# Kernel tuning notes

Hardware: AMD Instinct MI355X
Metric: run time of the kernel (lower is better)

## Reference

```python
import jax, jax.numpy as jnp
import numpy as np

B, T, D, H = 8192, 128, 16, 32
EPS = 1e-5  # BatchNorm1d default eps (eval mode, running stats)


def setup_inputs() -> dict:
    key = jax.random.key(0)
    ks = iter(jax.random.split(key, 64))

    def nrm(shape, s=0.1):
        return jax.random.normal(next(ks), shape, jnp.float32) * s

    inp = {}
    inp["S"] = nrm((B, T, D), 1.0)
    inp["g_S"] = nrm((B, T), 1.0)
    inp["times"] = jnp.linspace(0.0, 1.0, T, dtype=jnp.float32)
    inp["payoff_T"] = nrm((B,), 1.0)
    inp["delta_T"] = nrm((B, D), 1.0)
    # init_hidden: uniform(-0.1, 0.1), shape [num_layers=2, B, H]
    inp["h_price0"] = jax.random.uniform(next(ks), (2, B, H), jnp.float32, -0.1, 0.1)
    inp["h_delta0"] = jax.random.uniform(next(ks), (2, B, H), jnp.float32, -0.1, 0.1)
    # params for price net (prefix p_, out_dim=1) and delta net (prefix d_, out_dim=D)
    for pfx, out_dim in (("p", 1), ("d", D)):
        inp[pfx + "_Wih0"] = nrm((3 * H, 2 * D))
        inp[pfx + "_Whh0"] = nrm((3 * H, H))
        inp[pfx + "_bih0"] = nrm((3 * H,))
        inp[pfx + "_bhh0"] = nrm((3 * H,))
        inp[pfx + "_Wih1"] = nrm((3 * H, H))
        inp[pfx + "_Whh1"] = nrm((3 * H, H))
        inp[pfx + "_bih1"] = nrm((3 * H,))
        inp[pfx + "_bhh1"] = nrm((3 * H,))
        inp[pfx + "_embW"] = nrm((H, H))
        inp[pfx + "_embB"] = nrm((H,))
        inp[pfx + "_bng"] = jnp.ones((H,), jnp.float32)
        inp[pfx + "_bnb"] = jnp.zeros((H,), jnp.float32)
        inp[pfx + "_bnm"] = nrm((H,))
        inp[pfx + "_bnv"] = jax.random.uniform(next(ks), (H,), jnp.float32, 0.5, 1.5)
        inp[pfx + "_outW"] = nrm((out_dim, H))
        inp[pfx + "_outB"] = nrm((out_dim,))
    return inp


def _gru_cell(x, h, Wih, Whh, bih, bhh):
    # PyTorch GRU cell, gate order (r, z, n)
    gi = x @ Wih.T + bih
    gh = h @ Whh.T + bhh
    ir, iz, inn = jnp.split(gi, 3, axis=-1)
    hr, hz, hn = jnp.split(gh, 3, axis=-1)
    r = jax.nn.sigmoid(ir + hr)
    z = jax.nn.sigmoid(iz + hz)
    n = jnp.tanh(inn + r * hn)
    return (1.0 - z) * n + z * h


def _head(y, Wemb, bemb, g, b, m, v, Wout, bout, sig):
    # Linear -> BatchNorm1d (eval, running stats) -> SiLU -> Linear [-> Sigmoid]
    e = y @ Wemb.T + bemb
    e = (e - m) * jax.lax.rsqrt(v + EPS) * g + b
    e = e * jax.nn.sigmoid(e)  # SiLU
    o = e @ Wout.T + bout
    return jax.nn.sigmoid(o) if sig else o


def reference(S, g_S, times, payoff_T, delta_T, h_price0, h_delta0,
              p_Wih0, p_Whh0, p_bih0, p_bhh0, p_Wih1, p_Whh1, p_bih1, p_bhh1,
              p_embW, p_embB, p_bng, p_bnb, p_bnm, p_bnv, p_outW, p_outB,
              d_Wih0, d_Whh0, d_bih0, d_bhh0, d_Wih1, d_Whh1, d_bih1, d_bhh1,
              d_embW, d_embB, d_bng, d_bnb, d_bnm, d_bnv, d_outW, d_outB):
    # X = cat([S, g_S expanded to d]) -> [B, T, 2D]
    gS = jnp.broadcast_to(g_S[..., None], S.shape)
    X = jnp.concatenate([S, gS], axis=-1)
    Xr = jnp.swapaxes(X, 0, 1)[::-1]  # [T, B, 2D], time reversed (loop goes t=T-1..0)

    def step(carry, xt):
        hp0, hp1, hd0, hd1 = carry
        hp0 = _gru_cell(xt, hp0, p_Wih0, p_Whh0, p_bih0, p_bhh0)
        hp1 = _gru_cell(hp0, hp1, p_Wih1, p_Whh1, p_bih1, p_bhh1)
        hd0 = _gru_cell(xt, hd0, d_Wih0, d_Whh0, d_bih0, d_bhh0)
        hd1 = _gru_cell(hd0, hd1, d_Wih1, d_Whh1, d_bih1, d_bhh1)
        return (hp0, hp1, hd0, hd1), (hp1, hd1)

    carry0 = (h_price0[0], h_price0[1], h_delta0[0], h_delta0[1])
    _, (Yp, Yd) = jax.lax.scan(step, carry0, Xr)
    # flip time back to forward order: outputs were collected for t=T-1..0
    Yp = jnp.swapaxes(Yp[::-1], 0, 1)  # [B, T, H]
    Yd = jnp.swapaxes(Yd[::-1], 0, 1)  # [B, T, H]
    prices = _head(Yp, p_embW, p_embB, p_bng, p_bnb, p_bnm, p_bnv, p_outW, p_outB, False)  # [B,T,1]
    deltas = _head(Yd, d_embW, d_embB, d_bng, d_bnb, d_bnm, d_bnv, d_outW, d_outB, True)   # [B,T,D]
    return (prices, deltas)
```

## Files before the change

### kernel.cpp

```cpp
#include <hip/hip_runtime.h>
#include <hip/hip_bf16.h>
#include <stdint.h>

#define DI __device__ __forceinline__

typedef float f32x4 __attribute__((ext_vector_type(4)));
typedef short bf16x8 __attribute__((ext_vector_type(8)));

constexpr int BB = 8192, TT = 128, DD = 16, HH = 32;
constexpr float kEPS = 1e-5f;
constexpr float kLOG2E = 1.44269504088896340736f;

DI float rcpf_(float x) { return __builtin_amdgcn_rcpf(x); }
DI float exp2f_(float x) { return __builtin_amdgcn_exp2f(x); }
DI float sig_pre(float acc) { return rcpf_(1.0f + exp2f_(acc)); }
DI float sigm(float x) { return rcpf_(1.0f + exp2f_(-kLOG2E * x)); }

DI uint32_t cvtpk(float lo, float hi) {
  uint32_t r;
  asm("v_cvt_pk_bf16_f32 %0, %1, %2" : "=v"(r) : "v"(lo), "v"(hi));
  return r;
}

DI f32x4 mfma_(bf16x8 a, bf16x8 b, f32x4 c) {
  return __builtin_amdgcn_mfma_f32_16x16x32_bf16(a, b, c, 0, 0, 0);
}

DI void barrier_lds() {
  asm volatile("s_waitcnt lgkmcnt(0)" ::: "memory");
  __builtin_amdgcn_s_barrier();
  asm volatile("" ::: "memory");
}

union U4 { uint4 q; bf16x8 v; };

__global__ void prep_net(const float* Wih0, const float* Whh0,
                         const float* bih0, const float* bhh0,
                         const float* Wih1, const float* Whh1,
                         const float* bih1, const float* bhh1,
                         const float* embW, const float* embB,
                         const float* bng, const float* bnb,
                         const float* bnm, const float* bnv,
                         const float* outW, const float* outB,
                         int outDim, uint8_t* wsbase) {
  int tid = threadIdx.x;
  uint16_t* W = (uint16_t*)wsbase;
  float* bias = (float*)(wsbase + 27648);
  auto cvt = [](float f) -> uint16_t {
    union { float f; uint32_t u; } v; v.f = f;
    uint32_t u = v.u;
    return (uint16_t)((u + 0x7FFF + ((u >> 16) & 1)) >> 16);
  };
  for (int idx = tid; idx < 27 * 64; idx += 256) {
    int tile = idx >> 6, l = idx & 63, cc = l & 15, gg = l >> 4;
    uint16_t* dst = W + (size_t)idx * 8;
    if (tile < 24) {
      const float* mats[4] = {Wih0, Whh0, Wih1, Whh1};
      const float* src = mats[tile / 6];
      int sub = tile % 6;
      int row = sub * 16 + cc;
      float sc = (sub < 4) ? -kLOG2E : 2.0f * kLOG2E;
#pragma unroll
      for (int j = 0; j < 8; ++j) dst[j] = cvt(src[row * 32 + 8 * gg + j] * sc);
    } else if (tile < 26) {
      int row = (tile - 24) * 16 + cc;
      float a = bng[row] * rsqrtf(bnv[row] + kEPS);
#pragma unroll
      for (int j = 0; j < 8; ++j) dst[j] = cvt(embW[row * 32 + 8 * gg + j] * a);
    } else {
      int rrow = (cc < outDim) ? cc : 0;
      float sc = (cc < outDim) ? 1.0f : 0.0f;
#pragma unroll
      for (int j = 0; j < 8; ++j) dst[j] = cvt(outW[rrow * 32 + 8 * gg + j] * sc);
    }
  }
  for (int idx = tid; idx < 304; idx += 256) {
    int tile = idx >> 4, n = idx & 15;
    float v;
    if (tile < 8) {
      if (tile < 4)      v = (bih0[tile * 16 + n] + bhh0[tile * 16 + n]) * (-kLOG2E);
      else if (tile < 6) v = bih0[64 + (tile - 4) * 16 + n] * (2.0f * kLOG2E);
      else               v = bhh0[64 + (tile - 6) * 16 + n] * (2.0f * kLOG2E);
    } else if (tile < 16) {
      int tt = tile - 8;
      if (tt < 4)        v = (bih1[tt * 16 + n] + bhh1[tt * 16 + n]) * (-kLOG2E);
      else if (tt < 6)   v = bih1[64 + (tt - 4) * 16 + n] * (2.0f * kLOG2E);
      else               v = bhh1[64 + (tt - 6) * 16 + n] * (2.0f * kLOG2E);
    } else if (tile < 18) {
      int nn = (tile - 16) * 16 + n;
      float a = bng[nn] * rsqrtf(bnv[nn] + kEPS);
      v = a * (embB[nn] - bnm[nn]) + bnb[nn];
    } else {
      v = (n < outDim) ? outB[n] : 0.0f;
    }
    bias[idx] = v;
  }
}

__global__ __launch_bounds__(128, 2) void rnn_fused(
    const float* __restrict__ S, const float* __restrict__ gS,
    const float* __restrict__ hp0, const float* __restrict__ hd0,
    const uint8_t* __restrict__ ws, float* __restrict__ out) {
  const int tid = threadIdx.x, lane = tid & 63, wid = tid >> 6;
  const int net = blockIdx.x & 1;
  const int b0 = (blockIdx.x >> 1) * 16;
  const int c = lane & 15, g = lane >> 4;

  const uint16_t* W = (const uint16_t*)(ws + net * 32768);
  const float* bias = (const float*)(ws + net * 32768 + 27648);
  const float* hsrc = net ? hd0 : hp0;

  __shared__ uint4 sl[2][64];

  const int addr0 = ((lane & 15) | ((lane & 16) << 1)) << 2;
  const int addr1 = addr0 + 64;
  const bool lo32 = lane < 32;
  auto regroup = [&](const float (&v)[8]) -> bf16x8 {
    int P0 = (int)cvtpk(v[0], v[1]), P1 = (int)cvtpk(v[2], v[3]);
    int Q0 = (int)cvtpk(v[4], v[5]), Q1 = (int)cvtpk(v[6], v[7]);
    union { uint32_t u[4]; bf16x8 r; } t;
    int a, b;
    a = __builtin_amdgcn_ds_bpermute(addr0, P0);
    b = __builtin_amdgcn_ds_bpermute(addr0, Q0);
    t.u[0] = lo32 ? a : b;
    a = __builtin_amdgcn_ds_bpermute(addr0, P1);
    b = __builtin_amdgcn_ds_bpermute(addr0, Q1);
    t.u[1] = lo32 ? a : b;
    a = __builtin_amdgcn_ds_bpermute(addr1, P0);
    b = __builtin_amdgcn_ds_bpermute(addr1, Q0);
    t.u[2] = lo32 ? a : b;
    a = __builtin_amdgcn_ds_bpermute(addr1, P1);
    b = __builtin_amdgcn_ds_bpermute(addr1, Q1);
    t.u[3] = lo32 ? a : b;
    return t.r;
  };

  auto gruStep = [&](const bf16x8 (&Wi)[6], const bf16x8 (&Wh)[6],
                     const f32x4 (&Bb)[8], bf16x8 xf, bf16x8 hf,
                     float (&hC)[8]) {
    f32x4 r0 = mfma_(Wi[0], xf, Bb[0]); r0 = mfma_(Wh[0], hf, r0);
    f32x4 r1 = mfma_(Wi[1], xf, Bb[1]); r1 = mfma_(Wh[1], hf, r1);
    f32x4 z0 = mfma_(Wi[2], xf, Bb[2]); z0 = mfma_(Wh[2], hf, z0);
    f32x4 z1 = mfma_(Wi[3], xf, Bb[3]); z1 = mfma_(Wh[3], hf, z1);
    f32x4 ni0 = mfma_(Wi[4], xf, Bb[4]);
    f32x4 ni1 = mfma_(Wi[5], xf, Bb[5]);
    f32x4 nh0 = mfma_(Wh[4], hf, Bb[6]);
    f32x4 nh1 = mfma_(Wh[5], hf, Bb[7]);
#pragma unroll
    for (int r = 0; r < 4; ++r) {
      float rg0 = sig_pre(r0[r]), rg1 = sig_pre(r1[r]);
      float zg0 = sig_pre(z0[r]), zg1 = sig_pre(z1[r]);
      float w0 = ni0[r] + rg0 * nh0[r];
      float w1 = ni1[r] + rg1 * nh1[r];
      float n0 = 1.0f - 2.0f * rcpf_(1.0f + exp2f_(w0));
      float n1 = 1.0f - 2.0f * rcpf_(1.0f + exp2f_(w1));
      hC[r]     = n0 + zg0 * (hC[r]     - n0);
      hC[4 + r] = n1 + zg1 * (hC[4 + r] - n1);
    }
  };

  auto mkB = [&](const float* row) -> bf16x8 {
    f32x4 a = *(const f32x4*)(row);
    f32x4 b = *(const f32x4*)(row + 4);
    union { uint32_t u[4]; bf16x8 v; } t;
    t.u[0] = cvtpk(a[0], a[1]); t.u[1] = cvtpk(a[2], a[3]);
    t.u[2] = cvtpk(b[0], b[1]); t.u[3] = cvtpk(b[2], b[3]);
    return t.v;
  };

  if (wid == 0) {
    bf16x8 Wi[6], Wh[6];
#pragma unroll
    for (int t = 0; t < 6; ++t) {
      Wi[t] = *(const bf16x8*)(W + ((0 + t) * 64 + lane) * 8);
      Wh[t] = *(const bf16x8*)(W + ((6 + t) * 64 + lane) * 8);
    }
    f32x4 Bb[8];
#pragma unroll
    for (int t = 0; t < 8; ++t)
      Bb[t] = *(const f32x4*)(bias + t * 16 + 4 * g);

    float h0C[8];
#pragma unroll
    for (int r = 0; r < 4; ++r) {
      h0C[r]     = hsrc[(size_t)(b0 + c) * HH + 4 * g + r];
      h0C[4 + r] = hsrc[(size_t)(b0 + c) * HH + 16 + 4 * g + r];
    }
    bf16x8 h0B = mkB(hsrc + (size_t)(b0 + c) * HH + 8 * g);

    auto mkX = [&](f32x4 sa, f32x4 sb, float gs) -> bf16x8 {
      uint32_t pkg = cvtpk(gs, gs);
      union { uint32_t u[4]; bf16x8 v; } t;
      uint32_t p0 = cvtpk(sa[0], sa[1]), p1 = cvtpk(sa[2], sa[3]);
      uint32_t p2 = cvtpk(sb[0], sb[1]), p3 = cvtpk(sb[2], sb[3]);
      t.u[0] = lo32 ? p0 : pkg;
      t.u[1] = lo32 ? p1 : pkg;
      t.u[2] = lo32 ? p2 : pkg;
      t.u[3] = lo32 ? p3 : pkg;
      return t.v;
    };

    const float* Sp  = S  + ((size_t)(b0 + c) * TT + (TT - 1)) * DD + 8 * (g & 1);
    const float* gSp = gS + (size_t)(b0 + c) * TT + (TT - 1);
    f32x4 sa = *(const f32x4*)Sp, sb = *(const f32x4*)(Sp + 4);
    float gs = *gSp;

    bf16x8 xB = mkX(sa, sb, gs);
    gruStep(Wi, Wh, Bb, xB, h0B, h0C);
    h0B = regroup(h0C);
    { U4 u; u.v = h0B; sl[0][lane] = u.q; }
    Sp -= DD; gSp -= 1;
    sa = *(const f32x4*)Sp; sb = *(const f32x4*)(Sp + 4); gs = *gSp;
    barrier_lds();

#pragma unroll 1
    for (int i = 1; i < TT; ++i) {
      xB = mkX(sa, sb, gs);
      const float* Spn  = (i < TT - 1) ? Sp - DD : Sp;
      const float* gSpn = (i < TT - 1) ? gSp - 1 : gSp;
      sa = *(const f32x4*)Spn; sb = *(const f32x4*)(Spn + 4); gs = *gSpn;
      Sp = Spn; gSp = gSpn;

      gruStep(Wi, Wh, Bb, xB, h0B, h0C);
      h0B = regroup(h0C);
      { U4 u; u.v = h0B; sl[i & 1][lane] = u.q; }
      barrier_lds();
    }
  } else {
    bf16x8 Wi[6], Wh[6], We0, We1, Wo;
#pragma unroll
    for (int t = 0; t < 6; ++t) {
      Wi[t] = *(const bf16x8*)(W + ((12 + t) * 64 + lane) * 8);
      Wh[t] = *(const bf16x8*)(W + ((18 + t) * 64 + lane) * 8);
    }
    We0 = *(const bf16x8*)(W + (24 * 64 + lane) * 8);
    We1 = *(const bf16x8*)(W + (25 * 64 + lane) * 8);
    Wo  = *(const bf16x8*)(W + (26 * 64 + lane) * 8);
    f32x4 Bb[8];
#pragma unroll
    for (int t = 0; t < 8; ++t)
      Bb[t] = *(const f32x4*)(bias + (8 + t) * 16 + 4 * g);
    const f32x4 Be0 = *(const f32x4*)(bias + 16 * 16 + 4 * g);
    const f32x4 Be1 = *(const f32x4*)(bias + 17 * 16 + 4 * g);
    const f32x4 Bo  = *(const f32x4*)(bias + 18 * 16 + 4 * g);

    float h1C[8];
#pragma unroll
    for (int r = 0; r < 4; ++r) {
      h1C[r]     = hsrc[((size_t)BB + b0 + c) * HH + 4 * g + r];
      h1C[4 + r] = hsrc[((size_t)BB + b0 + c) * HH + 16 + 4 * g + r];
    }
    bf16x8 h1B = mkB(hsrc + ((size_t)BB + b0 + c) * HH + 8 * g);

    auto head = [&](bf16x8 h1f, int th) {
      f32x4 e0 = mfma_(We0, h1f, Be0);
      f32x4 e1 = mfma_(We1, h1f, Be1);
      float es[8];
#pragma unroll
      for (int r = 0; r < 4; ++r) {
        float a = e0[r], b = e1[r];
        es[r]     = a * sigm(a);
        es[4 + r] = b * sigm(b);
      }
      bf16x8 ef = regroup(es);
      f32x4 o = mfma_(Wo, ef, Bo);
      if (net == 0) {
        if (lane < 16) out[(size_t)(b0 + c) * TT + th] = o[0];
      } else {
        f32x4 so;
#pragma unroll
        for (int r = 0; r < 4; ++r) so[r] = sigm(o[r]);
        *(f32x4*)(out + (size_t)BB * TT +
                  ((size_t)(b0 + c) * TT + th) * DD + 4 * g) = so;
      }
    };

    barrier_lds();
#pragma unroll 1
    for (int i = 1; i < TT; ++i) {
      U4 u; u.q = sl[(i - 1) & 1][lane];
      bf16x8 h0t = u.v;
      gruStep(Wi, Wh, Bb, h0t, h1B, h1C);
      h1B = regroup(h1C);
      head(h1B, TT - i);
      barrier_lds();
    }
    U4 u; u.q = sl[1][lane];
    gruStep(Wi, Wh, Bb, u.v, h1B, h1C);
    h1B = regroup(h1C);
    head(h1B, 0);
  }
}

extern "C" void kernel_launch(void* const* d_in, const int* in_sizes, int n_in,
                              void* d_out, int out_size, void* d_ws,
                              size_t ws_size, hipStream_t stream) {
  const float* S   = (const float*)d_in[0];
  const float* gS  = (const float*)d_in[1];
  const float* hp0 = (const float*)d_in[5];
  const float* hd0 = (const float*)d_in[6];
  uint8_t* ws = (uint8_t*)d_ws;

  prep_net<<<1, 256, 0, stream>>>(
      (const float*)d_in[7],  (const float*)d_in[8],  (const float*)d_in[9],
      (const float*)d_in[10], (const float*)d_in[11], (const float*)d_in[12],
      (const float*)d_in[13], (const float*)d_in[14], (const float*)d_in[15],
      (const float*)d_in[16], (const float*)d_in[17], (const float*)d_in[18],
      (const float*)d_in[19], (const float*)d_in[20], (const float*)d_in[21],
      (const float*)d_in[22], 1, ws);
  prep_net<<<1, 256, 0, stream>>>(
      (const float*)d_in[23], (const float*)d_in[24], (const float*)d_in[25],
      (const float*)d_in[26], (const float*)d_in[27], (const float*)d_in[28],
      (const float*)d_in[29], (const float*)d_in[30], (const float*)d_in[31],
      (const float*)d_in[32], (const float*)d_in[33], (const float*)d_in[34],
      (const float*)d_in[35], (const float*)d_in[36], (const float*)d_in[37],
      (const float*)d_in[38], 16, ws + 32768);

  rnn_fused<<<dim3((BB / 16) * 2), dim3(128), 0, stream>>>(S, gS, hp0, hd0,
                                                           ws, (float*)d_out);
}
```

Baseline: 157.3 us.

## Split GRU layers and head into three warp-specialized pipeline stages with LDS rings

The block grows from two to three wavefronts. Wave 0 runs layer 0, wave 1 runs layer 1, and a new wave 2 runs the embedding/BN/SiLU/output head. They hand data through 8-deep LDS ring buffers. Each stage processes four timesteps between barriers, so there are fewer barriers and the head's matmuls and stores come off the layer-1 critical path. Wave 0 also batches its S and gS loads for four steps at once. The cost is more threads per block and more LDS, which changes occupancy, plus a two-epoch pipeline fill and drain.

```diff
diff --git a/kernel.cpp b/kernel.cpp
--- a/kernel.cpp
+++ b/kernel.cpp
@@ -97,7 +97,9 @@
   }
 }
 
-__global__ __launch_bounds__(128, 2) void rnn_fused(
+constexpr int KE = 4;
+constexpr int NE = TT / KE;
+__global__ __launch_bounds__(192, 3) void rnn_fused(
     const float* __restrict__ S, const float* __restrict__ gS,
     const float* __restrict__ hp0, const float* __restrict__ hd0,
     const uint8_t* __restrict__ ws, float* __restrict__ out) {
@@ -110,7 +112,8 @@
   const float* bias = (const float*)(ws + net * 32768 + 27648);
   const float* hsrc = net ? hd0 : hp0;
 
-  __shared__ uint4 sl[2][64];
+  __shared__ uint4 ring0[8][64];
+  __shared__ uint4 ring1[8][64];
 
   const int addr0 = ((lane & 15) | ((lane & 16) << 1)) << 2;
   const int addr1 = addr0 + 64;
@@ -200,57 +203,76 @@
       return t.v;
     };
 
-    const float* Sp  = S  + ((size_t)(b0 + c) * TT + (TT - 1)) * DD + 8 * (g & 1);
-    const float* gSp = gS + (size_t)(b0 + c) * TT + (TT - 1);
-    f32x4 sa = *(const f32x4*)Sp, sb = *(const f32x4*)(Sp + 4);
-    float gs = *gSp;
-
-    bf16x8 xB = mkX(sa, sb, gs);
-    gruStep(Wi, Wh, Bb, xB, h0B, h0C);
-    h0B = regroup(h0C);
-    { U4 u; u.v = h0B; sl[0][lane] = u.q; }
-    Sp -= DD; gSp -= 1;
-    sa = *(const f32x4*)Sp; sb = *(const f32x4*)(Sp + 4); gs = *gSp;
-    barrier_lds();
+    const float* Sbase  = S  + (size_t)(b0 + c) * TT * DD + 8 * (g & 1);
+    const float* gSbase = gS + (size_t)(b0 + c) * TT;
 
 #pragma unroll 1
-    for (int i = 1; i < TT; ++i) {
-      xB = mkX(sa, sb, gs);
-      const float* Spn  = (i < TT - 1) ? Sp - DD : Sp;
-      const float* gSpn = (i < TT - 1) ? gSp - 1 : gSp;
-      sa = *(const f32x4*)Spn; sb = *(const f32x4*)(Spn + 4); gs = *gSpn;
-      Sp = Spn; gSp = gSpn;
-
-      gruStep(Wi, Wh, Bb, xB, h0B, h0C);
-      h0B = regroup(h0C);
-      { U4 u; u.v = h0B; sl[i & 1][lane] = u.q; }
+    for (int e = 0; e < NE + 2; ++e) {
+      if (e < NE) {
+        const int sg0 = KE * e;
+        f32x4 sa[KE], sb[KE];
+        float gv[KE];
+#pragma unroll
+        for (int s = 0; s < KE; ++s) {
+          int t = TT - 1 - (sg0 + s);
+          const float* p = Sbase + (size_t)t * DD;
+          sa[s] = *(const f32x4*)p;
+          sb[s] = *(const f32x4*)(p + 4);
+          gv[s] = gSbase[t];
+        }
+#pragma unroll
+        for (int s = 0; s < KE; ++s) {
+          bf16x8 xB = mkX(sa[s], sb[s], gv[s]);
+          gruStep(Wi, Wh, Bb, xB, h0B, h0C);
+          h0B = regroup(h0C);
+          U4 u; u.v = h0B;
+          ring0[(sg0 + s) & 7][lane] = u.q;
+        }
+      }
       barrier_lds();
     }
-  } else {
-    bf16x8 Wi[6], Wh[6], We0, We1, Wo;
+  } else if (wid == 1) {
+    bf16x8 Wi[6], Wh[6];
 #pragma unroll
     for (int t = 0; t < 6; ++t) {
       Wi[t] = *(const bf16x8*)(W + ((12 + t) * 64 + lane) * 8);
       Wh[t] = *(const bf16x8*)(W + ((18 + t) * 64 + lane) * 8);
     }
-    We0 = *(const bf16x8*)(W + (24 * 64 + lane) * 8);
-    We1 = *(const bf16x8*)(W + (25 * 64 + lane) * 8);
-    Wo  = *(const bf16x8*)(W + (26 * 64 + lane) * 8);
     f32x4 Bb[8];
 #pragma unroll
     for (int t = 0; t < 8; ++t)
       Bb[t] = *(const f32x4*)(bias + (8 + t) * 16 + 4 * g);
+
+    float h1C[8];
+#pragma unroll
+    for (int r = 0; r < 4; ++r) {
+      h1C[r]     = hsrc[((size_t)BB + b0 + c) * HH + 4 * g + r];
+      h1C[4 + r] = hsrc[((size_t)BB + b0 + c) * HH + 16 + 4 * g + r];
+    }
+    bf16x8 h1B = mkB(hsrc + ((size_t)BB + b0 + c) * HH + 8 * g);
+
+#pragma unroll 1
+    for (int e = 0; e < NE + 2; ++e) {
+      if (e >= 1 && e <= NE) {
+        const int sg0 = KE * (e - 1);
+#pragma unroll
+        for (int s = 0; s < KE; ++s) {
+          U4 u; u.q = ring0[(sg0 + s) & 7][lane];
+          gruStep(Wi, Wh, Bb, u.v, h1B, h1C);
+          h1B = regroup(h1C);
+          U4 w; w.v = h1B;
+          ring1[(sg0 + s) & 7][lane] = w.q;
+        }
+      }
+      barrier_lds();
+    }
+  } else {
+    bf16x8 We0 = *(const bf16x8*)(W + (24 * 64 + lane) * 8);
+    bf16x8 We1 = *(const bf16x8*)(W + (25 * 64 + lane) * 8);
+    bf16x8 Wo  = *(const bf16x8*)(W + (26 * 64 + lane) * 8);
     const f32x4 Be0 = *(const f32x4*)(bias + 16 * 16 + 4 * g);
     const f32x4 Be1 = *(const f32x4*)(bias + 17 * 16 + 4 * g);
     const f32x4 Bo  = *(const f32x4*)(bias + 18 * 16 + 4 * g);
-
-    float h1C[8];
-#pragma unroll
-    for (int r = 0; r < 4; ++r) {
-      h1C[r]     = hsrc[((size_t)BB + b0 + c) * HH + 4 * g + r];
-      h1C[4 + r] = hsrc[((size_t)BB + b0 + c) * HH + 16 + 4 * g + r];
-    }
-    bf16x8 h1B = mkB(hsrc + ((size_t)BB + b0 + c) * HH + 8 * g);
 
     auto head = [&](bf16x8 h1f, int th) {
       f32x4 e0 = mfma_(We0, h1f, Be0);
@@ -275,20 +297,18 @@
       }
     };
 
-    barrier_lds();
 #pragma unroll 1
-    for (int i = 1; i < TT; ++i) {
-      U4 u; u.q = sl[(i - 1) & 1][lane];
-      bf16x8 h0t = u.v;
-      gruStep(Wi, Wh, Bb, h0t, h1B, h1C);
-      h1B = regroup(h1C);
-      head(h1B, TT - i);
+    for (int e = 0; e < NE + 2; ++e) {
+      if (e >= 2) {
+        const int sg0 = KE * (e - 2);
+#pragma unroll
+        for (int s = 0; s < KE; ++s) {
+          U4 u; u.q = ring1[(sg0 + s) & 7][lane];
+          head(u.v, TT - 1 - (sg0 + s));
+        }
+      }
       barrier_lds();
     }
-    U4 u; u.q = sl[1][lane];
-    gruStep(Wi, Wh, Bb, u.v, h1B, h1C);
-    h1B = regroup(h1C);
-    head(h1B, 0);
   }
 }
 
@@ -316,6 +336,6 @@
       (const float*)d_in[35], (const float*)d_in[36], (const float*)d_in[37],
       (const float*)d_in[38], 16, ws + 32768);
 
-  rnn_fused<<<dim3((BB / 16) * 2), dim3(128), 0, stream>>>(S, gS, hp0, hd0,
+  rnn_fused<<<dim3((BB / 16) * 2), dim3(192), 0, stream>>>(S, gS, hp0, hd0,
                                                            ws, (float*)d_out);
 }
```

Measured after the change: 162.8 us. 1.03x slower.

## Replace per-step barriers with flag-based 8-deep LDS ring between layer waves

Applied to the files above, without the earlier changes.

Layer-0 and layer-1 waves previously lockstepped via s_barrier on a 2-slot LDS buffer. They now communicate through an 8-entry LDS ring with volatile progress flags and sleep-polling, so the producer can run ahead of the consumer. The change also double-buffers the S/gS prefetch two steps ahead, and delays the head computation so it overlaps the next GRU step. The risks are polling overhead and memory-ordering correctness, since it relies on volatile LDS flags plus lgkmcnt waits.

```diff
diff --git a/kernel.cpp b/kernel.cpp
--- a/kernel.cpp
+++ b/kernel.cpp
@@ -24,12 +24,6 @@
 
 DI f32x4 mfma_(bf16x8 a, bf16x8 b, f32x4 c) {
   return __builtin_amdgcn_mfma_f32_16x16x32_bf16(a, b, c, 0, 0, 0);
-}
-
-DI void barrier_lds() {
-  asm volatile("s_waitcnt lgkmcnt(0)" ::: "memory");
-  __builtin_amdgcn_s_barrier();
-  asm volatile("" ::: "memory");
 }
 
 union U4 { uint4 q; bf16x8 v; };
@@ -110,7 +104,15 @@
   const float* bias = (const float*)(ws + net * 32768 + 27648);
   const float* hsrc = net ? hd0 : hp0;
 
-  __shared__ uint4 sl[2][64];
+  __shared__ uint4 ring0[8][64];
+  __shared__ volatile int flags[2];
+  if (tid < 2) flags[tid] = 0;
+  __syncthreads();
+
+  auto waitGE = [&](int idx, int target) {
+    if (flags[idx] >= target) return;
+    do { __builtin_amdgcn_s_sleep(1); } while (flags[idx] < target);
+  };
 
   const int addr0 = ((lane & 15) | ((lane & 16) << 1)) << 2;
   const int addr1 = addr0 + 64;
@@ -188,8 +190,8 @@
     }
     bf16x8 h0B = mkB(hsrc + (size_t)(b0 + c) * HH + 8 * g);
 
-    auto mkX = [&](f32x4 sa, f32x4 sb, float gs) -> bf16x8 {
-      uint32_t pkg = cvtpk(gs, gs);
+    auto mkX = [&](f32x4 sa, f32x4 sb, float gsv) -> bf16x8 {
+      uint32_t pkg = cvtpk(gsv, gsv);
       union { uint32_t u[4]; bf16x8 v; } t;
       uint32_t p0 = cvtpk(sa[0], sa[1]), p1 = cvtpk(sa[2], sa[3]);
       uint32_t p2 = cvtpk(sb[0], sb[1]), p3 = cvtpk(sb[2], sb[3]);
@@ -200,31 +202,35 @@
       return t.v;
     };
 
-    const float* Sp  = S  + ((size_t)(b0 + c) * TT + (TT - 1)) * DD + 8 * (g & 1);
-    const float* gSp = gS + (size_t)(b0 + c) * TT + (TT - 1);
-    f32x4 sa = *(const f32x4*)Sp, sb = *(const f32x4*)(Sp + 4);
-    float gs = *gSp;
-
-    bf16x8 xB = mkX(sa, sb, gs);
-    gruStep(Wi, Wh, Bb, xB, h0B, h0C);
-    h0B = regroup(h0C);
-    { U4 u; u.v = h0B; sl[0][lane] = u.q; }
-    Sp -= DD; gSp -= 1;
-    sa = *(const f32x4*)Sp; sb = *(const f32x4*)(Sp + 4); gs = *gSp;
-    barrier_lds();
-
-#pragma unroll 1
-    for (int i = 1; i < TT; ++i) {
-      xB = mkX(sa, sb, gs);
-      const float* Spn  = (i < TT - 1) ? Sp - DD : Sp;
-      const float* gSpn = (i < TT - 1) ? gSp - 1 : gSp;
-      sa = *(const f32x4*)Spn; sb = *(const f32x4*)(Spn + 4); gs = *gSpn;
-      Sp = Spn; gSp = gSpn;
-
+    const float* Sbase  = S  + (size_t)(b0 + c) * TT * DD + 8 * (g & 1);
+    const float* gSbase = gS + (size_t)(b0 + c) * TT;
+
+    f32x4 sa0 = *(const f32x4*)(Sbase + (size_t)(TT - 1) * DD);
+    f32x4 sb0 = *(const f32x4*)(Sbase + (size_t)(TT - 1) * DD + 4);
+    float gv0 = gSbase[TT - 1];
+    f32x4 sa1 = *(const f32x4*)(Sbase + (size_t)(TT - 2) * DD);
+    f32x4 sb1 = *(const f32x4*)(Sbase + (size_t)(TT - 2) * DD + 4);
+    float gv1 = gSbase[TT - 2];
+
+#pragma unroll 2
+    for (int i = 0; i < TT; ++i) {
+      int tn = TT - 3 - i; if (tn < 0) tn = 0;
+      const float* p = Sbase + (size_t)tn * DD;
+      f32x4 san = *(const f32x4*)p, sbn = *(const f32x4*)(p + 4);
+      float gvn = gSbase[tn];
+
+      bf16x8 xB = mkX(sa0, sb0, gv0);
       gruStep(Wi, Wh, Bb, xB, h0B, h0C);
       h0B = regroup(h0C);
-      { U4 u; u.v = h0B; sl[i & 1][lane] = u.q; }
-      barrier_lds();
+
+      if (i >= 7) waitGE(1, i - 7);
+      asm volatile("" ::: "memory");
+      { U4 u; u.v = h0B; ring0[i & 7][lane] = u.q; }
+      asm volatile("s_waitcnt lgkmcnt(0)" ::: "memory");
+      if (lane == 0) flags[0] = i + 1;
+
+      sa0 = sa1; sb0 = sb1; gv0 = gv1;
+      sa1 = san; sb1 = sbn; gv1 = gvn;
     }
   } else {
     bf16x8 Wi[6], Wh[6], We0, We1, Wo;
@@ -275,19 +281,19 @@
       }
     };
 
-    barrier_lds();
 #pragma unroll 1
-    for (int i = 1; i < TT; ++i) {
-      U4 u; u.q = sl[(i - 1) & 1][lane];
-      bf16x8 h0t = u.v;
-      gruStep(Wi, Wh, Bb, h0t, h1B, h1C);
+    for (int i = 0; i < TT; ++i) {
+      waitGE(0, i + 1);
+      asm volatile("" ::: "memory");
+      U4 u; u.q = ring0[i & 7][lane];
+      asm volatile("s_waitcnt lgkmcnt(0)" ::: "memory");
+      if (lane == 0) flags[1] = i + 1;
+
+      bf16x8 h1prev = h1B;
+      gruStep(Wi, Wh, Bb, u.v, h1B, h1C);
+      if (i > 0) head(h1prev, TT - i);
       h1B = regroup(h1C);
-      head(h1B, TT - i);
-      barrier_lds();
-    }
-    U4 u; u.q = sl[1][lane];
-    gruStep(Wi, Wh, Bb, u.v, h1B, h1C);
-    h1B = regroup(h1C);
+    }
     head(h1B, 0);
   }
 }
```

After: 162.0 us. 1.03x slower.
